# Kernel tuning notes

Hardware: AMD Instinct MI355X
Metric: run time of the kernel (lower is better)

Reference implementation:

```python
import jax, jax.numpy as jnp
import numpy as np

B, H, W, DIM = 64, 28, 28, 384
N = B * H * W
E, K, R = 3, 2, 8
HID = 4 * DIM
SCALING = 8.0 / 8.0  # alpha / r


def setup_inputs() -> dict:
    key = jax.random.key(0)
    ks = jax.random.split(key, 8)
    x = jax.random.normal(ks[0], (B, H, W, DIM), dtype=jnp.float32)
    gate = jax.random.uniform(ks[1], (N, E), dtype=jnp.float32)
    topk_probs = jax.random.uniform(ks[2], (N, K), dtype=jnp.float32)
    topk_idx = jax.random.randint(ks[3], (N, K), 0, E)
    # LoRA expert params (w_up is zeros in the original init; use small randn
    # so the MoE path is numerically non-trivial for kernel testing)
    w_down = jax.random.normal(ks[4], (E, DIM, R), dtype=jnp.float32) * (1.0 / DIM ** 0.5)
    w_up = jax.random.normal(ks[5], (E, R, DIM), dtype=jnp.float32) * 0.02
    # frozen base ConvNeXt MLP: Linear(dim,4dim) -> GELU -> Linear(4dim,dim)
    W1 = jax.random.normal(ks[6], (DIM, HID), dtype=jnp.float32) * 0.02
    b1 = jnp.zeros((HID,), dtype=jnp.float32)
    W2 = jax.random.normal(ks[7], (HID, DIM), dtype=jnp.float32) * 0.02
    b2 = jnp.zeros((DIM,), dtype=jnp.float32)
    return {"x": x, "gate": gate, "topk_probs": topk_probs, "topk_idx": topk_idx,
            "w_down": w_down, "w_up": w_up, "W1": W1, "b1": b1, "W2": W2, "b2": b2}


def reference(x, gate, topk_probs, topk_idx, w_down, w_up, W1, b1, W2, b2):
    gelu = lambda t: jax.nn.gelu(t, approximate=False)  # torch nn.GELU() default = exact erf
    # frozen base MLP
    orig = gelu(jnp.einsum('bhwd,df->bhwf', x, W1) + b1)
    orig = jnp.einsum('bhwf,fd->bhwd', orig, W2) + b2
    # MoE LoRA path over flattened tokens
    x_flat = x.reshape(-1, x.shape[-1])          # [N, dim]
    moe = jnp.zeros_like(x_flat)
    n_experts = w_down.shape[0]
    for i in range(n_experts):
        # combined routing weight for expert i (0 for tokens not routed here)
        prob = jnp.sum(jnp.where(topk_idx == i, topk_probs, 0.0), axis=1)  # [N]
        out_i = gelu(x_flat @ w_down[i]) @ w_up[i] * SCALING               # [N, dim]
        moe = moe + out_i * prob[:, None]
    return orig + moe.reshape(x.shape)
```

## Files before the change

### kernel.cpp

```cpp
#include <hip/hip_runtime.h>
#include <hip/hip_bf16.h>

typedef __attribute__((ext_vector_type(4))) float float4v;
typedef __attribute__((ext_vector_type(8))) __bf16 bf16x8;
typedef __attribute__((ext_vector_type(8))) unsigned short ushort8v;

constexpr int NTOK = 50176;
constexpr int DIM  = 384;
constexpr int HID  = 1536;
constexpr int BM   = 64;
constexpr int NTH  = 512;
constexpr int NBLK = NTOK / BM;
constexpr int CHW  = 32;
constexpr int NCH  = HID / CHW;

constexpr int IMG_WD  = 0;
constexpr int IMG_WUP = 24576;
constexpr int IMG_W1  = 49152;
constexpr int IMG_W2  = 49152 + 48 * 24576;
constexpr size_t WS_NEED = 2408448;
constexpr int NELEMS = 1204224;

constexpr int L_X  = 0;
constexpr int L_W  = 49152;
constexpr int L_HS = 73728;
constexpr int LDSZ = 77824;

__device__ __forceinline__ unsigned short f2bf(float f) {
  __hip_bfloat16 h = __float2bfloat16(f);
  return *reinterpret_cast<unsigned short*>(&h);
}

__device__ __forceinline__ float gelu_f(float v) {
  float u = 0.7978845608f * (v + 0.044715f * v * v * v);
  float e = __expf(2.0f * u);
  float t = 1.0f - 2.0f / (e + 1.0f);
  return 0.5f * v * (1.0f + t);
}

__device__ __forceinline__ void stage3(const char* src, char* dst, int tid) {
  ushort8v t0 = *(const ushort8v*)(src + tid * 16);
  ushort8v t1 = *(const ushort8v*)(src + tid * 16 + 8192);
  ushort8v t2 = *(const ushort8v*)(src + tid * 16 + 16384);
  *(ushort8v*)(dst + tid * 16)         = t0;
  *(ushort8v*)(dst + tid * 16 + 8192)  = t1;
  *(ushort8v*)(dst + tid * 16 + 16384) = t2;
}

__global__ __launch_bounds__(256) void pack_k(
    const float* __restrict__ W1, const float* __restrict__ W2,
    const float* __restrict__ wd, const float* __restrict__ wu,
    unsigned short* __restrict__ img)
{
  int i = blockIdx.x * 256 + threadIdx.x;
  if (i >= NELEMS) return;
  if (i < 12288) {
    int f = i / 384; int inb = (i % 384) * 2;
    int d = (inb ^ ((f & 7) << 4)) >> 1;
    float v = (f < 24) ? wd[(f >> 3) * (DIM * 8) + d * 8 + (f & 7)] : 0.f;
    img[i] = f2bf(v);
  } else if (i < 24576) {
    int j = i - 12288;
    int d = j / 32; int inb = (j % 32) * 2;
    int k = (inb ^ ((d & 3) << 4)) >> 1;
    float v = (k < 24) ? wu[k * DIM + d] : 0.f;
    img[i] = f2bf(v);
  } else if (i < 24576 + 48 * 12288) {
    int j = i - 24576; int h = j / 12288; int jc = j % 12288;
    int f = jc / 384; int inb = (jc % 384) * 2;
    int d = (inb ^ ((f & 7) << 4)) >> 1;
    img[i] = f2bf(W1[d * HID + h * CHW + f]);
  } else {
    int j = i - 24576 - 48 * 12288; int h = j / 12288; int jc = j % 12288;
    int d = jc / 32; int inb = (jc % 32) * 2;
    int k = (inb ^ ((d & 3) << 4)) >> 1;
    img[i] = f2bf(W2[(h * CHW + k) * DIM + d]);
  }
}

__global__ __launch_bounds__(NTH, 4) void fused_k(
    const float* __restrict__ x,
    const float* __restrict__ tp,
    const int*   __restrict__ ti,
    const float* __restrict__ b1,
    const float* __restrict__ b2,
    const unsigned short* __restrict__ img,
    float* __restrict__ out)
{
  extern __shared__ char lds[];
  const int tid = threadIdx.x, wid = tid >> 6, lane = tid & 63;
  const int lrow = lane & 15, g4 = lane >> 4, lkb = g4 * 8;
  const int blockRow = blockIdx.x * BM;
  const char* imgc = (const char*)img;

  const int band = wid >> 1, chh = wid & 1;
  const int wr = wid >> 2, wc = wid & 3;

  {
    const float* xb = x + (size_t)blockRow * DIM;
    #pragma unroll
    for (int it = 0; it < 6; ++it) {
      int idx = it * NTH + tid;
      int row = idx / 48, c8 = idx % 48;
      float4v v0 = *(const float4v*)(xb + row * DIM + c8 * 8);
      float4v v1 = *(const float4v*)(xb + row * DIM + c8 * 8 + 4);
      ushort8v u;
      u[0]=f2bf(v0[0]); u[1]=f2bf(v0[1]); u[2]=f2bf(v0[2]); u[3]=f2bf(v0[3]);
      u[4]=f2bf(v1[0]); u[5]=f2bf(v1[1]); u[6]=f2bf(v1[2]); u[7]=f2bf(v1[3]);
      int byte = (row * 768 + c8 * 16) ^ ((row & 7) << 4);
      *(ushort8v*)(lds + L_X + byte) = u;
    }
  }
  stage3(imgc + IMG_WD, lds + L_W, tid);
  __syncthreads();

  {
    float4v hv = {};
    int raX = band * 16 + lrow, swA = (raX & 7) << 4, baX = raX * 768 + lkb * 2;
    int rbW = chh * 16 + lrow, swB = (rbW & 7) << 4, baW = rbW * 768 + lkb * 2;
    #pragma unroll
    for (int ks = 0; ks < 12; ++ks) {
      bf16x8 a = *(const bf16x8*)(lds + L_X + ((baX + ks * 64) ^ swA));
      bf16x8 b = *(const bf16x8*)(lds + L_W + ((baW + ks * 64) ^ swB));
      hv = __builtin_amdgcn_mfma_f32_16x16x32_bf16(a, b, hv, 0, 0, 0);
    }
    int colc = chh * 16 + lrow; int e = colc >> 3;
    #pragma unroll
    for (int r = 0; r < 4; ++r) {
      int row = band * 16 + g4 * 4 + r;
      int token = blockRow + row;
      float p = 0.f;
      if (e < 3) {
        int i0 = ti[token * 2], i1 = ti[token * 2 + 1];
        if (i0 == e) p += tp[token * 2];
        if (i1 == e) p += tp[token * 2 + 1];
      }
      float gv = p * gelu_f(hv[r]);
      int byte = (row * 64) + ((colc * 2) ^ ((row & 3) << 4));
      *(unsigned short*)(lds + L_HS + byte) = f2bf(gv);
    }
  }
  __syncthreads();
  stage3(imgc + IMG_WUP, lds + L_W, tid);
  __syncthreads();

  float4v acc[2][6] = {};
  {
    bf16x8 A[2];
    #pragma unroll
    for (int mt = 0; mt < 2; ++mt) {
      int ra = wr * 32 + mt * 16 + lrow;
      A[mt] = *(const bf16x8*)(lds + L_HS + ra * 64 + ((g4 * 16) ^ ((ra & 3) << 4)));
    }
    #pragma unroll
    for (int nt = 0; nt < 6; ++nt) {
      int rd = wc * 96 + nt * 16 + lrow;
      bf16x8 b = *(const bf16x8*)(lds + L_W + rd * 64 + ((g4 * 16) ^ ((rd & 3) << 4)));
      acc[0][nt] = __builtin_amdgcn_mfma_f32_16x16x32_bf16(A[0], b, acc[0][nt], 0, 0, 0);
      acc[1][nt] = __builtin_amdgcn_mfma_f32_16x16x32_bf16(A[1], b, acc[1][nt], 0, 0, 0);
    }
  }

  for (int h = 0; h < NCH; ++h) {
    __syncthreads();
    stage3(imgc + IMG_W1 + h * 24576, lds + L_W, tid);
    __syncthreads();

    float4v hv = {};
    {
      int raX = band * 16 + lrow, swA = (raX & 7) << 4, baX = raX * 768 + lkb * 2;
      int rbW = chh * 16 + lrow, swB = (rbW & 7) << 4, baW = rbW * 768 + lkb * 2;
      #pragma unroll
      for (int ks = 0; ks < 12; ++ks) {
        bf16x8 a = *(const bf16x8*)(lds + L_X + ((baX + ks * 64) ^ swA));
        bf16x8 b = *(const bf16x8*)(lds + L_W + ((baW + ks * 64) ^ swB));
        hv = __builtin_amdgcn_mfma_f32_16x16x32_bf16(a, b, hv, 0, 0, 0);
      }
    }
    {
      int colc = chh * 16 + lrow;
      float bb = b1[h * CHW + colc];
      #pragma unroll
      for (int r = 0; r < 4; ++r) {
        int row = band * 16 + g4 * 4 + r;
        float gv = gelu_f(hv[r] + bb);
        int byte = (row * 64) + ((colc * 2) ^ ((row & 3) << 4));
        *(unsigned short*)(lds + L_HS + byte) = f2bf(gv);
      }
    }
    __syncthreads();
    stage3(imgc + IMG_W2 + h * 24576, lds + L_W, tid);
    __syncthreads();

    {
      bf16x8 A[2];
      #pragma unroll
      for (int mt = 0; mt < 2; ++mt) {
        int ra = wr * 32 + mt * 16 + lrow;
        A[mt] = *(const bf16x8*)(lds + L_HS + ra * 64 + ((g4 * 16) ^ ((ra & 3) << 4)));
      }
      #pragma unroll
      for (int nt = 0; nt < 6; ++nt) {
        int rd = wc * 96 + nt * 16 + lrow;
        bf16x8 b = *(const bf16x8*)(lds + L_W + rd * 64 + ((g4 * 16) ^ ((rd & 3) << 4)));
        acc[0][nt] = __builtin_amdgcn_mfma_f32_16x16x32_bf16(A[0], b, acc[0][nt], 0, 0, 0);
        acc[1][nt] = __builtin_amdgcn_mfma_f32_16x16x32_bf16(A[1], b, acc[1][nt], 0, 0, 0);
      }
    }
  }

  #pragma unroll
  for (int nt = 0; nt < 6; ++nt) {
    int col = wc * 96 + nt * 16 + lrow;
    float bb = b2[col];
    #pragma unroll
    for (int mt = 0; mt < 2; ++mt) {
      #pragma unroll
      for (int r = 0; r < 4; ++r) {
        int row = wr * 32 + mt * 16 + g4 * 4 + r;
        out[(size_t)(blockRow + row) * DIM + col] = acc[mt][nt][r] + bb;
      }
    }
  }
}

extern "C" void kernel_launch(void* const* d_in, const int* in_sizes, int n_in,
                              void* d_out, int out_size, void* d_ws, size_t ws_size,
                              hipStream_t stream) {
  const float* x          = (const float*)d_in[0];
  const float* topk_probs = (const float*)d_in[2];
  const int*   topk_idx   = (const int*)  d_in[3];
  const float* w_down     = (const float*)d_in[4];
  const float* w_up       = (const float*)d_in[5];
  const float* W1         = (const float*)d_in[6];
  const float* b1         = (const float*)d_in[7];
  const float* W2         = (const float*)d_in[8];
  const float* b2         = (const float*)d_in[9];
  float* out = (float*)d_out;

  if (ws_size < WS_NEED) return;

  hipFuncSetAttribute(reinterpret_cast<const void*>(fused_k),
                      hipFuncAttributeMaxDynamicSharedMemorySize, LDSZ);

  unsigned short* img = (unsigned short*)d_ws;
  pack_k<<<(NELEMS + 255) / 256, 256, 0, stream>>>(W1, W2, w_down, w_up, img);
  fused_k<<<NBLK, NTH, LDSZ, stream>>>(x, topk_probs, topk_idx, b1, b2, img, out);
}
```

Baseline: 327.3 us.

## Read weight fragments directly from global memory and widen hidden chunks to 64

Stops staging W1/W2 and LoRA weight chunks through LDS and has each wave load its MFMA B fragments straight from global/L2 in a plain, unswizzled packed layout. The hidden chunk width doubles to 64, which halves the number of chunk iterations and block-wide barriers. Each wave now computes 32x16 tiles for the first GEMM. This removes the LDS copy and two syncs per chunk and frees LDS for higher occupancy. In exchange, every wave repeats global loads of the same weight fragments, so performance depends on L2/L1 hit rates and load latency that is no longer hidden by staging.

New measurement: 572.5 us. 74.9% more time.

```diff
diff --git a/kernel.cpp b/kernel.cpp
--- a/kernel.cpp
+++ b/kernel.cpp
@@ -11,20 +11,19 @@
 constexpr int BM   = 64;
 constexpr int NTH  = 512;
 constexpr int NBLK = NTOK / BM;
-constexpr int CHW  = 32;
+constexpr int CHW  = 64;
 constexpr int NCH  = HID / CHW;
 
-constexpr int IMG_WD  = 0;
-constexpr int IMG_WUP = 24576;
-constexpr int IMG_W1  = 49152;
-constexpr int IMG_W2  = 49152 + 48 * 24576;
+constexpr int IMG_W1P = 0;
+constexpr int IMG_W2P = 1179648;
+constexpr int IMG_WD  = 2359296;
+constexpr int IMG_WUP = 2383872;
 constexpr size_t WS_NEED = 2408448;
 constexpr int NELEMS = 1204224;
 
 constexpr int L_X  = 0;
-constexpr int L_W  = 49152;
-constexpr int L_HS = 73728;
-constexpr int LDSZ = 77824;
+constexpr int L_HS = 49152;
+constexpr int LDSZ = 57344;
 
 __device__ __forceinline__ unsigned short f2bf(float f) {
   __hip_bfloat16 h = __float2bfloat16(f);
@@ -36,15 +35,6 @@
   float e = __expf(2.0f * u);
   float t = 1.0f - 2.0f / (e + 1.0f);
   return 0.5f * v * (1.0f + t);
-}
-
-__device__ __forceinline__ void stage3(const char* src, char* dst, int tid) {
-  ushort8v t0 = *(const ushort8v*)(src + tid * 16);
-  ushort8v t1 = *(const ushort8v*)(src + tid * 16 + 8192);
-  ushort8v t2 = *(const ushort8v*)(src + tid * 16 + 16384);
-  *(ushort8v*)(dst + tid * 16)         = t0;
-  *(ushort8v*)(dst + tid * 16 + 8192)  = t1;
-  *(ushort8v*)(dst + tid * 16 + 16384) = t2;
 }
 
 __global__ __launch_bounds__(256) void pack_k(
@@ -54,27 +44,23 @@
 {
   int i = blockIdx.x * 256 + threadIdx.x;
   if (i >= NELEMS) return;
-  if (i < 12288) {
-    int f = i / 384; int inb = (i % 384) * 2;
-    int d = (inb ^ ((f & 7) << 4)) >> 1;
-    float v = (f < 24) ? wd[(f >> 3) * (DIM * 8) + d * 8 + (f & 7)] : 0.f;
+  if (i < 589824) {
+    int f = i / 384, d = i % 384;
+    img[i] = f2bf(W1[d * HID + f]);
+  } else if (i < 1179648) {
+    int j = i - 589824;
+    int d = j / 1536, k = j % 1536;
+    img[i] = f2bf(W2[k * DIM + d]);
+  } else if (i < 1179648 + 12288) {
+    int j = i - 1179648;
+    int c = j / 384, d = j % 384;
+    float v = (c < 24) ? wd[(c >> 3) * (DIM * 8) + d * 8 + (c & 7)] : 0.f;
     img[i] = f2bf(v);
-  } else if (i < 24576) {
-    int j = i - 12288;
-    int d = j / 32; int inb = (j % 32) * 2;
-    int k = (inb ^ ((d & 3) << 4)) >> 1;
-    float v = (k < 24) ? wu[k * DIM + d] : 0.f;
+  } else {
+    int j = i - 1191936;
+    int d = j / 32, c = j % 32;
+    float v = (c < 24) ? wu[c * DIM + d] : 0.f;
     img[i] = f2bf(v);
-  } else if (i < 24576 + 48 * 12288) {
-    int j = i - 24576; int h = j / 12288; int jc = j % 12288;
-    int f = jc / 384; int inb = (jc % 384) * 2;
-    int d = (inb ^ ((f & 7) << 4)) >> 1;
-    img[i] = f2bf(W1[d * HID + h * CHW + f]);
-  } else {
-    int j = i - 24576 - 48 * 12288; int h = j / 12288; int jc = j % 12288;
-    int d = jc / 32; int inb = (jc % 32) * 2;
-    int k = (inb ^ ((d & 3) << 4)) >> 1;
-    img[i] = f2bf(W2[(h * CHW + k) * DIM + d]);
   }
 }
 
@@ -89,11 +75,10 @@
 {
   extern __shared__ char lds[];
   const int tid = threadIdx.x, wid = tid >> 6, lane = tid & 63;
-  const int lrow = lane & 15, g4 = lane >> 4, lkb = g4 * 8;
+  const int lrow = lane & 15, g4 = lane >> 4;
   const int blockRow = blockIdx.x * BM;
   const char* imgc = (const char*)img;
 
-  const int band = wid >> 1, chh = wid & 1;
   const int wr = wid >> 2, wc = wid & 3;
 
   {
@@ -111,37 +96,43 @@
       *(ushort8v*)(lds + L_X + byte) = u;
     }
   }
-  stage3(imgc + IMG_WD, lds + L_W, tid);
   __syncthreads();
 
+  float4v hv[2] = {};
+  if (wc < 2) {
+    const char* bsrc = imgc + IMG_WD + (wc * 16 + lrow) * 768 + g4 * 16;
+    int ar0 = wr * 32 + lrow, ar1 = ar0 + 16;
+    int s0 = (ar0 & 7) << 4, s1 = (ar1 & 7) << 4;
+    int ab0 = ar0 * 768 + g4 * 16, ab1 = ar1 * 768 + g4 * 16;
+    #pragma unroll
+    for (int ks = 0; ks < 12; ++ks) {
+      bf16x8 a0 = *(const bf16x8*)(lds + L_X + ((ab0 + ks * 64) ^ s0));
+      bf16x8 a1 = *(const bf16x8*)(lds + L_X + ((ab1 + ks * 64) ^ s1));
+      bf16x8 b  = *(const bf16x8*)(bsrc + ks * 64);
+      hv[0] = __builtin_amdgcn_mfma_f32_16x16x32_bf16(a0, b, hv[0], 0, 0, 0);
+      hv[1] = __builtin_amdgcn_mfma_f32_16x16x32_bf16(a1, b, hv[1], 0, 0, 0);
+    }
+  }
   {
-    float4v hv = {};
-    int raX = band * 16 + lrow, swA = (raX & 7) << 4, baX = raX * 768 + lkb * 2;
-    int rbW = chh * 16 + lrow, swB = (rbW & 7) << 4, baW = rbW * 768 + lkb * 2;
-    #pragma unroll
-    for (int ks = 0; ks < 12; ++ks) {
-      bf16x8 a = *(const bf16x8*)(lds + L_X + ((baX + ks * 64) ^ swA));
-      bf16x8 b = *(const bf16x8*)(lds + L_W + ((baW + ks * 64) ^ swB));
-      hv = __builtin_amdgcn_mfma_f32_16x16x32_bf16(a, b, hv, 0, 0, 0);
-    }
-    int colc = chh * 16 + lrow; int e = colc >> 3;
-    #pragma unroll
-    for (int r = 0; r < 4; ++r) {
-      int row = band * 16 + g4 * 4 + r;
-      int token = blockRow + row;
-      float p = 0.f;
-      if (e < 3) {
-        int i0 = ti[token * 2], i1 = ti[token * 2 + 1];
-        if (i0 == e) p += tp[token * 2];
-        if (i1 == e) p += tp[token * 2 + 1];
-      }
-      float gv = p * gelu_f(hv[r]);
-      int byte = (row * 64) + ((colc * 2) ^ ((row & 3) << 4));
-      *(unsigned short*)(lds + L_HS + byte) = f2bf(gv);
-    }
-  }
-  __syncthreads();
-  stage3(imgc + IMG_WUP, lds + L_W, tid);
+    int col = wc * 16 + lrow; int e = col >> 3;
+    #pragma unroll
+    for (int mt = 0; mt < 2; ++mt) {
+      #pragma unroll
+      for (int r = 0; r < 4; ++r) {
+        int row = wr * 32 + mt * 16 + g4 * 4 + r;
+        int token = blockRow + row;
+        float p = 0.f;
+        if (e < 3) {
+          int i0 = ti[token * 2], i1 = ti[token * 2 + 1];
+          if (i0 == e) p += tp[token * 2];
+          if (i1 == e) p += tp[token * 2 + 1];
+        }
+        float gv = p * gelu_f(hv[mt][r]);
+        int byte = (row * 128 + col * 2) ^ ((row & 7) << 4);
+        *(unsigned short*)(lds + L_HS + byte) = f2bf(gv);
+      }
+    }
+  }
   __syncthreads();
 
   float4v acc[2][6] = {};
@@ -150,12 +141,12 @@
     #pragma unroll
     for (int mt = 0; mt < 2; ++mt) {
       int ra = wr * 32 + mt * 16 + lrow;
-      A[mt] = *(const bf16x8*)(lds + L_HS + ra * 64 + ((g4 * 16) ^ ((ra & 3) << 4)));
+      A[mt] = *(const bf16x8*)(lds + L_HS + ra * 128 + ((g4 * 16) ^ ((ra & 7) << 4)));
     }
     #pragma unroll
     for (int nt = 0; nt < 6; ++nt) {
       int rd = wc * 96 + nt * 16 + lrow;
-      bf16x8 b = *(const bf16x8*)(lds + L_W + rd * 64 + ((g4 * 16) ^ ((rd & 3) << 4)));
+      bf16x8 b = *(const bf16x8*)(imgc + IMG_WUP + rd * 64 + g4 * 16);
       acc[0][nt] = __builtin_amdgcn_mfma_f32_16x16x32_bf16(A[0], b, acc[0][nt], 0, 0, 0);
       acc[1][nt] = __builtin_amdgcn_mfma_f32_16x16x32_bf16(A[1], b, acc[1][nt], 0, 0, 0);
     }
@@ -163,46 +154,50 @@
 
   for (int h = 0; h < NCH; ++h) {
     __syncthreads();
-    stage3(imgc + IMG_W1 + h * 24576, lds + L_W, tid);
+
+    float4v hg[2] = {};
+    {
+      const char* bsrc = imgc + IMG_W1P + (size_t)(h * 64 + wc * 16 + lrow) * 768 + g4 * 16;
+      int ar0 = wr * 32 + lrow, ar1 = ar0 + 16;
+      int s0 = (ar0 & 7) << 4, s1 = (ar1 & 7) << 4;
+      int ab0 = ar0 * 768 + g4 * 16, ab1 = ar1 * 768 + g4 * 16;
+      #pragma unroll
+      for (int ks = 0; ks < 12; ++ks) {
+        bf16x8 a0 = *(const bf16x8*)(lds + L_X + ((ab0 + ks * 64) ^ s0));
+        bf16x8 a1 = *(const bf16x8*)(lds + L_X + ((ab1 + ks * 64) ^ s1));
+        bf16x8 b  = *(const bf16x8*)(bsrc + ks * 64);
+        hg[0] = __builtin_amdgcn_mfma_f32_16x16x32_bf16(a0, b, hg[0], 0, 0, 0);
+        hg[1] = __builtin_amdgcn_mfma_f32_16x16x32_bf16(a1, b, hg[1], 0, 0, 0);
+      }
+    }
+    {
+      int col = wc * 16 + lrow;
+      float bb = b1[h * 64 + col];
+      #pragma unroll
+      for (int mt = 0; mt < 2; ++mt) {
+        #pragma unroll
+        for (int r = 0; r < 4; ++r) {
+          int row = wr * 32 + mt * 16 + g4 * 4 + r;
+          float gv = gelu_f(hg[mt][r] + bb);
+          int byte = (row * 128 + col * 2) ^ ((row & 7) << 4);
+          *(unsigned short*)(lds + L_HS + byte) = f2bf(gv);
+        }
+      }
+    }
     __syncthreads();
 
-    float4v hv = {};
-    {
-      int raX = band * 16 + lrow, swA = (raX & 7) << 4, baX = raX * 768 + lkb * 2;
-      int rbW = chh * 16 + lrow, swB = (rbW & 7) << 4, baW = rbW * 768 + lkb * 2;
-      #pragma unroll
-      for (int ks = 0; ks < 12; ++ks) {
-        bf16x8 a = *(const bf16x8*)(lds + L_X + ((baX + ks * 64) ^ swA));
-        bf16x8 b = *(const bf16x8*)(lds + L_W + ((baW + ks * 64) ^ swB));
-        hv = __builtin_amdgcn_mfma_f32_16x16x32_bf16(a, b, hv, 0, 0, 0);
-      }
-    }
-    {
-      int colc = chh * 16 + lrow;
-      float bb = b1[h * CHW + colc];
-      #pragma unroll
-      for (int r = 0; r < 4; ++r) {
-        int row = band * 16 + g4 * 4 + r;
-        float gv = gelu_f(hv[r] + bb);
-        int byte = (row * 64) + ((colc * 2) ^ ((row & 3) << 4));
-        *(unsigned short*)(lds + L_HS + byte) = f2bf(gv);
-      }
-    }
-    __syncthreads();
-    stage3(imgc + IMG_W2 + h * 24576, lds + L_W, tid);
-    __syncthreads();
-
-    {
+    #pragma unroll
+    for (int kk = 0; kk < 2; ++kk) {
       bf16x8 A[2];
       #pragma unroll
       for (int mt = 0; mt < 2; ++mt) {
         int ra = wr * 32 + mt * 16 + lrow;
-        A[mt] = *(const bf16x8*)(lds + L_HS + ra * 64 + ((g4 * 16) ^ ((ra & 3) << 4)));
+        A[mt] = *(const bf16x8*)(lds + L_HS + ra * 128 + ((kk * 64 + g4 * 16) ^ ((ra & 7) << 4)));
       }
       #pragma unroll
       for (int nt = 0; nt < 6; ++nt) {
         int rd = wc * 96 + nt * 16 + lrow;
-        bf16x8 b = *(const bf16x8*)(lds + L_W + rd * 64 + ((g4 * 16) ^ ((rd & 3) << 4)));
+        bf16x8 b = *(const bf16x8*)(imgc + IMG_W2P + (size_t)rd * 3072 + (h * 64 + kk * 32 + g4 * 8) * 2);
         acc[0][nt] = __builtin_amdgcn_mfma_f32_16x16x32_bf16(A[0], b, acc[0][nt], 0, 0, 0);
         acc[1][nt] = __builtin_amdgcn_mfma_f32_16x16x32_bf16(A[1], b, acc[1][nt], 0, 0, 0);
       }
```

## Prefetch next weight chunk into registers and pad LDS rows instead of XOR swizzle

Applied to the files above, without the earlier changes.

Weight staging is split into a global-to-register load and a later register-to-LDS write, so the next chunk's global load is issued before the current compute phase and its latency is hidden behind MFMA work. The 32-wide hidden and W2 tiles switch from an XOR swizzle to 72-byte padded rows, which avoids bank conflicts with simpler address arithmetic but grows LDS to 81920 bytes. Holding the prefetched chunk adds live registers, and the larger LDS footprint could reduce occupancy below the 4 blocks per CU requested in the launch bounds.

Measured after the change: 670.2 us. +104.7%, slower.

```diff
diff --git a/kernel.cpp b/kernel.cpp
--- a/kernel.cpp
+++ b/kernel.cpp
@@ -23,8 +23,8 @@
 
 constexpr int L_X  = 0;
 constexpr int L_W  = 49152;
-constexpr int L_HS = 73728;
-constexpr int LDSZ = 77824;
+constexpr int L_HS = 76800;
+constexpr int LDSZ = 81920;
 
 __device__ __forceinline__ unsigned short f2bf(float f) {
   __hip_bfloat16 h = __float2bfloat16(f);
@@ -38,13 +38,22 @@
   return 0.5f * v * (1.0f + t);
 }
 
-__device__ __forceinline__ void stage3(const char* src, char* dst, int tid) {
-  ushort8v t0 = *(const ushort8v*)(src + tid * 16);
-  ushort8v t1 = *(const ushort8v*)(src + tid * 16 + 8192);
-  ushort8v t2 = *(const ushort8v*)(src + tid * 16 + 16384);
-  *(ushort8v*)(dst + tid * 16)         = t0;
-  *(ushort8v*)(dst + tid * 16 + 8192)  = t1;
-  *(ushort8v*)(dst + tid * 16 + 16384) = t2;
+__device__ __forceinline__ void st_load(const char* src, int tid, ushort8v st[3]) {
+  #pragma unroll
+  for (int j = 0; j < 3; ++j)
+    st[j] = *(const ushort8v*)(src + tid * 16 + j * 8192);
+}
+__device__ __forceinline__ void st_wr_lin(char* dst, int tid, const ushort8v st[3]) {
+  #pragma unroll
+  for (int j = 0; j < 3; ++j)
+    *(ushort8v*)(dst + tid * 16 + j * 8192) = st[j];
+}
+__device__ __forceinline__ void st_wr_pad(char* dst, int tid, const ushort8v st[3]) {
+  #pragma unroll
+  for (int j = 0; j < 3; ++j) {
+    int b = j * 8192 + tid * 16;
+    *(ushort8v*)(dst + (b >> 6) * 72 + (b & 63)) = st[j];
+  }
 }
 
 __global__ __launch_bounds__(256) void pack_k(
@@ -55,15 +64,14 @@
   int i = blockIdx.x * 256 + threadIdx.x;
   if (i >= NELEMS) return;
   if (i < 12288) {
-    int f = i / 384; int inb = (i % 384) * 2;
-    int d = (inb ^ ((f & 7) << 4)) >> 1;
-    float v = (f < 24) ? wd[(f >> 3) * (DIM * 8) + d * 8 + (f & 7)] : 0.f;
+    int r = i / 384; int inb = (i % 384) * 2;
+    int d = (inb ^ ((r & 7) << 4)) >> 1;
+    float v = (r < 24) ? wd[(r >> 3) * (DIM * 8) + d * 8 + (r & 7)] : 0.f;
     img[i] = f2bf(v);
   } else if (i < 24576) {
     int j = i - 12288;
-    int d = j / 32; int inb = (j % 32) * 2;
-    int k = (inb ^ ((d & 3) << 4)) >> 1;
-    float v = (k < 24) ? wu[k * DIM + d] : 0.f;
+    int d = j / 32, c = j % 32;
+    float v = (c < 24) ? wu[c * DIM + d] : 0.f;
     img[i] = f2bf(v);
   } else if (i < 24576 + 48 * 12288) {
     int j = i - 24576; int h = j / 12288; int jc = j % 12288;
@@ -72,8 +80,7 @@
     img[i] = f2bf(W1[d * HID + h * CHW + f]);
   } else {
     int j = i - 24576 - 48 * 12288; int h = j / 12288; int jc = j % 12288;
-    int d = jc / 32; int inb = (jc % 32) * 2;
-    int k = (inb ^ ((d & 3) << 4)) >> 1;
+    int d = jc / 32, k = jc % 32;
     img[i] = f2bf(W2[(h * CHW + k) * DIM + d]);
   }
 }
@@ -89,13 +96,16 @@
 {
   extern __shared__ char lds[];
   const int tid = threadIdx.x, wid = tid >> 6, lane = tid & 63;
-  const int lrow = lane & 15, g4 = lane >> 4, lkb = g4 * 8;
+  const int lrow = lane & 15, g4 = lane >> 4;
   const int blockRow = blockIdx.x * BM;
   const char* imgc = (const char*)img;
 
   const int band = wid >> 1, chh = wid & 1;
   const int wr = wid >> 2, wc = wid & 3;
 
+  ushort8v st[3];
+
+  st_load(imgc + IMG_WD, tid, st);
   {
     const float* xb = x + (size_t)blockRow * DIM;
     #pragma unroll
@@ -111,17 +121,19 @@
       *(ushort8v*)(lds + L_X + byte) = u;
     }
   }
-  stage3(imgc + IMG_WD, lds + L_W, tid);
+  __syncthreads();
+  st_wr_lin(lds + L_W, tid, st);
+  st_load(imgc + IMG_WUP, tid, st);
   __syncthreads();
 
   {
     float4v hv = {};
-    int raX = band * 16 + lrow, swA = (raX & 7) << 4, baX = raX * 768 + lkb * 2;
-    int rbW = chh * 16 + lrow, swB = (rbW & 7) << 4, baW = rbW * 768 + lkb * 2;
+    int raX = band * 16 + lrow, sA = (raX & 7) << 4, baX = raX * 768 + g4 * 16;
+    int rbW = chh * 16 + lrow, sB = (rbW & 7) << 4, baW = rbW * 768 + g4 * 16;
     #pragma unroll
     for (int ks = 0; ks < 12; ++ks) {
-      bf16x8 a = *(const bf16x8*)(lds + L_X + ((baX + ks * 64) ^ swA));
-      bf16x8 b = *(const bf16x8*)(lds + L_W + ((baW + ks * 64) ^ swB));
+      bf16x8 a = *(const bf16x8*)(lds + L_X + ((baX + ks * 64) ^ sA));
+      bf16x8 b = *(const bf16x8*)(lds + L_W + ((baW + ks * 64) ^ sB));
       hv = __builtin_amdgcn_mfma_f32_16x16x32_bf16(a, b, hv, 0, 0, 0);
     }
     int colc = chh * 16 + lrow; int e = colc >> 3;
@@ -136,12 +148,12 @@
         if (i1 == e) p += tp[token * 2 + 1];
       }
       float gv = p * gelu_f(hv[r]);
-      int byte = (row * 64) + ((colc * 2) ^ ((row & 3) << 4));
-      *(unsigned short*)(lds + L_HS + byte) = f2bf(gv);
-    }
-  }
-  __syncthreads();
-  stage3(imgc + IMG_WUP, lds + L_W, tid);
+      *(unsigned short*)(lds + L_HS + row * 72 + colc * 2) = f2bf(gv);
+    }
+  }
+  __syncthreads();
+  st_wr_pad(lds + L_W, tid, st);
+  st_load(imgc + IMG_W1, tid, st);
   __syncthreads();
 
   float4v acc[2][6] = {};
@@ -150,12 +162,12 @@
     #pragma unroll
     for (int mt = 0; mt < 2; ++mt) {
       int ra = wr * 32 + mt * 16 + lrow;
-      A[mt] = *(const bf16x8*)(lds + L_HS + ra * 64 + ((g4 * 16) ^ ((ra & 3) << 4)));
+      A[mt] = *(const bf16x8*)(lds + L_HS + ra * 72 + g4 * 16);
     }
     #pragma unroll
     for (int nt = 0; nt < 6; ++nt) {
       int rd = wc * 96 + nt * 16 + lrow;
-      bf16x8 b = *(const bf16x8*)(lds + L_W + rd * 64 + ((g4 * 16) ^ ((rd & 3) << 4)));
+      bf16x8 b = *(const bf16x8*)(lds + L_W + rd * 72 + g4 * 16);
       acc[0][nt] = __builtin_amdgcn_mfma_f32_16x16x32_bf16(A[0], b, acc[0][nt], 0, 0, 0);
       acc[1][nt] = __builtin_amdgcn_mfma_f32_16x16x32_bf16(A[1], b, acc[1][nt], 0, 0, 0);
     }
@@ -163,17 +175,18 @@
 
   for (int h = 0; h < NCH; ++h) {
     __syncthreads();
-    stage3(imgc + IMG_W1 + h * 24576, lds + L_W, tid);
+    st_wr_lin(lds + L_W, tid, st);
+    st_load(imgc + IMG_W2 + h * 24576, tid, st);
     __syncthreads();
 
     float4v hv = {};
     {
-      int raX = band * 16 + lrow, swA = (raX & 7) << 4, baX = raX * 768 + lkb * 2;
-      int rbW = chh * 16 + lrow, swB = (rbW & 7) << 4, baW = rbW * 768 + lkb * 2;
+      int raX = band * 16 + lrow, sA = (raX & 7) << 4, baX = raX * 768 + g4 * 16;
+      int rbW = chh * 16 + lrow, sB = (rbW & 7) << 4, baW = rbW * 768 + g4 * 16;
       #pragma unroll
       for (int ks = 0; ks < 12; ++ks) {
-        bf16x8 a = *(const bf16x8*)(lds + L_X + ((baX + ks * 64) ^ swA));
-        bf16x8 b = *(const bf16x8*)(lds + L_W + ((baW + ks * 64) ^ swB));
+        bf16x8 a = *(const bf16x8*)(lds + L_X + ((baX + ks * 64) ^ sA));
+        bf16x8 b = *(const bf16x8*)(lds + L_W + ((baW + ks * 64) ^ sB));
         hv = __builtin_amdgcn_mfma_f32_16x16x32_bf16(a, b, hv, 0, 0, 0);
       }
     }
@@ -184,12 +197,13 @@
       for (int r = 0; r < 4; ++r) {
         int row = band * 16 + g4 * 4 + r;
         float gv = gelu_f(hv[r] + bb);
-        int byte = (row * 64) + ((colc * 2) ^ ((row & 3) << 4));
-        *(unsigned short*)(lds + L_HS + byte) = f2bf(gv);
-      }
-    }
-    __syncthreads();
-    stage3(imgc + IMG_W2 + h * 24576, lds + L_W, tid);
+        *(unsigned short*)(lds + L_HS + row * 72 + colc * 2) = f2bf(gv);
+      }
+    }
+    __syncthreads();
+    st_wr_pad(lds + L_W, tid, st);
+    if (h < NCH - 1)
+      st_load(imgc + IMG_W1 + (h + 1) * 24576, tid, st);
     __syncthreads();
 
     {
@@ -197,12 +211,12 @@
       #pragma unroll
       for (int mt = 0; mt < 2; ++mt) {
         int ra = wr * 32 + mt * 16 + lrow;
-        A[mt] = *(const bf16x8*)(lds + L_HS + ra * 64 + ((g4 * 16) ^ ((ra & 3) << 4)));
+        A[mt] = *(const bf16x8*)(lds + L_HS + ra * 72 + g4 * 16);
       }
       #pragma unroll
       for (int nt = 0; nt < 6; ++nt) {
         int rd = wc * 96 + nt * 16 + lrow;
-        bf16x8 b = *(const bf16x8*)(lds + L_W + rd * 64 + ((g4 * 16) ^ ((rd & 3) << 4)));
+        bf16x8 b = *(const bf16x8*)(lds + L_W + rd * 72 + g4 * 16);
         acc[0][nt] = __builtin_amdgcn_mfma_f32_16x16x32_bf16(A[0], b, acc[0][nt], 0, 0, 0);
         acc[1][nt] = __builtin_amdgcn_mfma_f32_16x16x32_bf16(A[1], b, acc[1][nt], 0, 0, 0);
       }
```
